# Performance work log

Hardware: AMD Instinct MI355X
Metric: run time of the kernel (lower is better)

Reference implementation:

```python
import jax, jax.numpy as jnp
import numpy as np
from jax import lax

I, H, C = 1086, 16, 15


def _lstm_layer(x, w_ih, w_hh, b):
    # x: [B, T, in], w_ih: [4H, in], w_hh: [4H, H], b: [4H]  (b = b_ih + b_hh)
    B = x.shape[0]
    Hd = w_hh.shape[1]
    # precompute the big input projection outside the scan
    pre = jnp.einsum('bti,gi->btg', x, w_ih) + b  # [B, T, 4H]

    def step(carry, pt):
        h, c = carry
        gates = pt + h @ w_hh.T  # [B, 4H]
        i, f, g, o = jnp.split(gates, 4, axis=-1)  # torch gate order i,f,g,o
        i = jax.nn.sigmoid(i)
        f = jax.nn.sigmoid(f)
        g = jnp.tanh(g)
        o = jax.nn.sigmoid(o)
        c = f * c + i * g
        h = o * jnp.tanh(c)
        return (h, c), h

    h0 = jnp.zeros((B, Hd), x.dtype)
    c0 = jnp.zeros((B, Hd), x.dtype)
    _, ys = lax.scan(step, (h0, c0), jnp.swapaxes(pre, 0, 1))
    return jnp.swapaxes(ys, 0, 1)  # [B, T, H]


def setup_inputs() -> dict:
    key = jax.random.key(0)
    ks = jax.random.split(key, 20)
    s = 1.0 / np.sqrt(H)  # torch LSTM/Linear default init scale
    x = jax.random.normal(ks[0], (256, 200, I), dtype=jnp.float32)

    def w(k, shape):
        return jax.random.uniform(k, shape, jnp.float32, -s, s)

    inp = {'x': x}
    ins = [I, H, H, H]  # lstm1 layer0/1, lstm2 layer0/1
    names = ['l0a', 'l0b', 'l1a', 'l1b']
    ki = 1
    for n, d_in in zip(names, ins):
        inp['w_ih_' + n] = w(ks[ki], (4 * H, d_in)); ki += 1
        inp['w_hh_' + n] = w(ks[ki], (4 * H, H)); ki += 1
        inp['b_' + n] = w(ks[ki], (4 * H,)); ki += 1
    inp['w_fc1'] = w(ks[ki], (H, H)); ki += 1
    inp['b_fc1'] = w(ks[ki], (H,)); ki += 1
    inp['w_fc2'] = w(ks[ki], (C, H)); ki += 1
    inp['b_fc2'] = w(ks[ki], (C,))
    return inp


def reference(x, w_ih_l0a, w_hh_l0a, b_l0a, w_ih_l0b, w_hh_l0b, b_l0b,
              w_ih_l1a, w_hh_l1a, b_l1a, w_ih_l1b, w_hh_l1b, b_l1b,
              w_fc1, b_fc1, w_fc2, b_fc2):
    # lstm1 (2 layers), dropout between layers is identity in eval mode
    out = _lstm_layer(x, w_ih_l0a, w_hh_l0a, b_l0a)
    out = _lstm_layer(out, w_ih_l0b, w_hh_l0b, b_l0b)
    # lstm2 (2 layers)
    out = _lstm_layer(out, w_ih_l1a, w_hh_l1a, b_l1a)
    out = _lstm_layer(out, w_ih_l1b, w_hh_l1b, b_l1b)
    h_last = out[:, -1, :]  # [B, H]
    h = jax.nn.relu(h_last @ w_fc1.T + b_fc1)
    logits = h @ w_fc2.T + b_fc2  # [B, C]
    return jax.nn.softmax(logits, axis=1)
```

## Files before the change

### kernel.cpp

```cpp
#include <hip/hip_runtime.h>

#define T_STEPS 200
#define IN_DIM 1086
#define KTILES 34
#define M_TOTAL 51200

using f32x4v  = __attribute__((ext_vector_type(4))) float;
using bf16x8  = __attribute__((ext_vector_type(8))) short;
using u32x4   = __attribute__((ext_vector_type(4))) unsigned int;
typedef unsigned uv2 __attribute__((ext_vector_type(2)));

#if __has_builtin(__builtin_amdgcn_permlane16_swap) && __has_builtin(__builtin_amdgcn_permlane32_swap)
#define HAVE_PERMLANE_SWAP 1
#else
#define HAVE_PERMLANE_SWAP 0
#endif

#if __has_builtin(__builtin_amdgcn_exp2f)
#define EXP2F(x) __builtin_amdgcn_exp2f(x)
#else
#define EXP2F(x) exp2f(x)
#endif

#define GLDS(gp, lp, sz) __builtin_amdgcn_global_load_lds(                         \
    (const __attribute__((address_space(1))) unsigned int*)(gp),                   \
    (__attribute__((address_space(3))) unsigned int*)(lp), sz, 0, 0)

__device__ __forceinline__ float rl_f(float v, int lane) {
    return __uint_as_float((unsigned)__builtin_amdgcn_readlane((int)__float_as_uint(v), lane));
}

__global__ __launch_bounds__(256) void prepack_w(
    const float* __restrict__ W,
    unsigned short* __restrict__ Wh, unsigned short* __restrict__ Wl)
{
    int idx = blockIdx.x * 256 + threadIdx.x;
    if (idx >= KTILES * 4 * 64 * 8) return;
    int j = idx & 7;
    int n = (idx >> 3) & 63;
    int k = (idx >> 9) * 8 + j;
    float v = (k < IN_DIM) ? W[n * IN_DIM + k] : 0.0f;
    unsigned u = __float_as_uint(v);
    unsigned hi = u & 0xffff0000u;
    float lo = v - __uint_as_float(hi);
    Wh[idx] = (unsigned short)(u >> 16);
    Wl[idx] = (unsigned short)(__float_as_uint(lo) >> 16);
}

__device__ __forceinline__ void cvt_hilo(const float (&a)[8], bf16x8& hv, bf16x8& lv) {
    union { u32x4 u; bf16x8 v; } H, L;
    #pragma unroll
    for (int p = 0; p < 4; ++p) {
        float a0 = a[2 * p], a1 = a[2 * p + 1];
        unsigned u0 = __float_as_uint(a0), u1 = __float_as_uint(a1);
        unsigned h0 = u0 & 0xffff0000u, h1 = u1 & 0xffff0000u;
        H.u[p] = (u0 >> 16) | h1;
        float l0 = a0 - __uint_as_float(h0);
        float l1 = a1 - __uint_as_float(h1);
        L.u[p] = (__float_as_uint(l0) >> 16) | (__float_as_uint(l1) & 0xffff0000u);
    }
    hv = H.v; lv = L.v;
}

__global__ __launch_bounds__(256) void pre0_gemm_v5(
    const float* __restrict__ X,
    const unsigned short* __restrict__ Wh, const unsigned short* __restrict__ Wl,
    const float* __restrict__ bias, float* __restrict__ out)
{
    __shared__ float          As[2][2048];
    __shared__ unsigned short Bs[2][2][2048];

    const int tid  = threadIdx.x;
    const int lane = tid & 63;
    const int wv   = tid >> 6;
    const int fr   = lane & 15;
    const int kg   = lane >> 4;
    const long m0  = (long)blockIdx.x * 64;

    const int rbase = wv * 16 + (lane >> 5);
    const int sidx  = (lane >> 2) & 7;
    const int dsub  = lane & 3;
    int koff[8];
    #pragma unroll
    for (int i = 0; i < 8; ++i)
        koff[i] = ((sidx ^ ((rbase + 2 * i) & 7)) * 4 + dsub) * 4;
    const char* Xrow = (const char*)X + (m0 + rbase) * 4344;

    f32x4v acc[4];
    #pragma unroll
    for (int nf = 0; nf < 4; ++nf)
        #pragma unroll
        for (int r = 0; r < 4; ++r) acc[nf][r] = 0.0f;

    {
        #pragma unroll
        for (int i = 0; i < 8; ++i) {
            int off = koff[i];
            GLDS(Xrow + (long)i * 8688 + off, &As[0][wv * 512 + i * 64], 4);
        }
        GLDS(Wh + tid * 8, (char*)Bs[0][0] + wv * 1024, 16);
        GLDS(Wl + tid * 8, (char*)Bs[0][1] + wv * 1024, 16);
    }

    for (int kt = 0; kt < KTILES; ++kt) {
        const int cur = kt & 1;
        __syncthreads();

        if (kt + 1 < KTILES) {
            const int nb = cur ^ 1, kb = (kt + 1) * 128;
            #pragma unroll
            for (int i = 0; i < 8; ++i) {
                int off = kb + koff[i];
                off = off > 4340 ? 4340 : off;
                GLDS(Xrow + (long)i * 8688 + off, &As[nb][wv * 512 + i * 64], 4);
            }
            GLDS(Wh + (size_t)(kt + 1) * 2048 + tid * 8, (char*)Bs[nb][0] + wv * 1024, 16);
            GLDS(Wl + (size_t)(kt + 1) * 2048 + tid * 8, (char*)Bs[nb][1] + wv * 1024, 16);
        }

        const int r  = wv * 16 + fr;
        const int r7 = r & 7;
        const float* pa1 = &As[cur][r * 32 + (((2 * kg) ^ r7) << 2)];
        const float* pa2 = &As[cur][r * 32 + ((((2 * kg) | 1) ^ r7) << 2)];
        float a[8];
        *(f32x4v*)&a[0] = *(const f32x4v*)pa1;
        *(f32x4v*)&a[4] = *(const f32x4v*)pa2;
        bf16x8 ah, al;
        cvt_hilo(a, ah, al);
        #pragma unroll
        for (int nf = 0; nf < 4; ++nf) {
            const int bofs = (kg * 64 + nf * 16 + fr) * 8;
            bf16x8 bh = *(const bf16x8*)&Bs[cur][0][bofs];
            bf16x8 bl = *(const bf16x8*)&Bs[cur][1][bofs];
            acc[nf] = __builtin_amdgcn_mfma_f32_16x16x32_bf16(ah, bh, acc[nf], 0, 0, 0);
            acc[nf] = __builtin_amdgcn_mfma_f32_16x16x32_bf16(al, bh, acc[nf], 0, 0, 0);
            acc[nf] = __builtin_amdgcn_mfma_f32_16x16x32_bf16(ah, bl, acc[nf], 0, 0, 0);
        }
    }

    float bvv[4];
    #pragma unroll
    for (int nf = 0; nf < 4; ++nf) bvv[nf] = bias[nf * 16 + fr];
    #pragma unroll
    for (int nf = 0; nf < 4; ++nf)
        #pragma unroll
        for (int rr = 0; rr < 4; ++rr) {
            long row = m0 + wv * 16 + kg * 4 + rr;
            out[row * 64 + nf * 16 + fr] = acc[nf][rr] + bvv[nf];
        }
}

__global__ __launch_bounds__(256) void mega_scan(
    const float* __restrict__ pre0, const float* __restrict__ whh0,
    const float* __restrict__ wih1, const float* __restrict__ whh1, const float* __restrict__ b1,
    const float* __restrict__ wih2, const float* __restrict__ whh2, const float* __restrict__ b2,
    const float* __restrict__ wih3, const float* __restrict__ whh3, const float* __restrict__ b3,
    const float* __restrict__ w_fc1, const float* __restrict__ b_fc1,
    const float* __restrict__ w_fc2, const float* __restrict__ b_fc2,
    float* __restrict__ out)
{
    __shared__ float buf[3][T_STEPS][16];

    const int b    = blockIdx.x;
    const int tid  = threadIdx.x;
    const int g    = tid & 63;
    const int wv   = tid >> 6;

    bool sel16 = false, sel32 = false;
#if HAVE_PERMLANE_SWAP
    {
        uv2 q16 = __builtin_amdgcn_permlane16_swap((unsigned)g, (unsigned)g, false, false);
        sel16 = (__builtin_amdgcn_readfirstlane((int)q16[1]) == 16);
        uv2 q32 = __builtin_amdgcn_permlane32_swap((unsigned)g, (unsigned)g, false, false);
        sel32 = (__builtin_amdgcn_readfirstlane((int)q32[1]) == 32);
    }
#endif

    const float* wih = nullptr; const float* whh; const float* bias = nullptr;
    if      (wv == 0) { whh = whh0; }
    else if (wv == 1) { wih = wih1; whh = whh1; bias = b1; }
    else if (wv == 2) { wih = wih2; whh = whh2; bias = b2; }
    else              { wih = wih3; whh = whh3; bias = b3; }

    float whh_r[16];
    #pragma unroll
    for (int q = 0; q < 4; ++q)
        *(float4*)&whh_r[q * 4] = *(const float4*)&whh[g * 16 + q * 4];
    float wih_r[16]; float bg = 0.0f;
    if (wv) {
        #pragma unroll
        for (int q = 0; q < 4; ++q)
            *(float4*)&wih_r[q * 4] = *(const float4*)&wih[g * 16 + q * 4];
        bg = bias[g];
    }

    const float* pb = pre0 + (size_t)b * T_STEPS * 64 + g;
    float pc = 0.0f, p1 = 0.0f, p2 = 0.0f;
    if (wv == 0) { pc = pb[0]; p1 = pb[64]; p2 = pb[128]; }

    float hs[16];
    #pragma unroll
    for (int k = 0; k < 16; ++k) hs[k] = 0.0f;
    float c = 0.0f;

    const int q4 = g >> 4;
    const float escale = (q4 == 2) ? -2.8853900817779268f : -1.4426950408889634f;
    const float am = (q4 == 2) ? 2.0f : 1.0f;
    const float aa = (q4 == 2) ? -1.0f : 0.0f;

    for (int tau = 0; tau < T_STEPS + 3; ++tau) {
        __syncthreads();
        const int t = tau - wv;
        if (t >= 0 && t < T_STEPS) {
            float xr[16];
            if (wv) {
                #pragma unroll
                for (int q = 0; q < 4; ++q)
                    *(float4*)&xr[q * 4] = *(const float4*)&buf[wv - 1][t][q * 4];
            }
            float r0 = fmaf(whh_r[0], hs[0], wv ? bg : pc);
            float r1 = whh_r[1] * hs[1];
            float r2 = whh_r[2] * hs[2];
            float r3 = whh_r[3] * hs[3];
            #pragma unroll
            for (int k = 4; k < 16; k += 4) {
                r0 = fmaf(whh_r[k + 0], hs[k + 0], r0);
                r1 = fmaf(whh_r[k + 1], hs[k + 1], r1);
                r2 = fmaf(whh_r[k + 2], hs[k + 2], r2);
                r3 = fmaf(whh_r[k + 3], hs[k + 3], r3);
            }
            float acc = (r0 + r1) + (r2 + r3);
            if (wv) {
                float p0 = wih_r[0] * xr[0];
                float q1 = wih_r[1] * xr[1];
                float q2 = wih_r[2] * xr[2];
                float q3 = wih_r[3] * xr[3];
                #pragma unroll
                for (int k = 4; k < 16; k += 4) {
                    p0 = fmaf(wih_r[k + 0], xr[k + 0], p0);
                    q1 = fmaf(wih_r[k + 1], xr[k + 1], q1);
                    q2 = fmaf(wih_r[k + 2], xr[k + 2], q2);
                    q3 = fmaf(wih_r[k + 3], xr[k + 3], q3);
                }
                acc += (p0 + q1) + (q2 + q3);
            }
            float e = EXP2F(escale * acc);
            float s = __builtin_amdgcn_rcpf(1.0f + e);
            float a = fmaf(am, s, aa);
#if HAVE_PERMLANE_SWAP
            unsigned au = __float_as_uint(a);
            uv2 r16 = __builtin_amdgcn_permlane16_swap(au, au, false, false);
            uv2 r32 = __builtin_amdgcn_permlane32_swap(au, au, false, false);
            unsigned fvu = sel16 ? r16[1] : r16[0];
            unsigned gvu = sel32 ? r32[1] : r32[0];
            uv2 r48 = __builtin_amdgcn_permlane16_swap(gvu, gvu, false, false);
            unsigned ovu = sel16 ? r48[1] : r48[0];
            float fv = __uint_as_float(fvu);
            float gv = __uint_as_float(gvu);
            float ov = __uint_as_float(ovu);
#else
            float fv = __shfl_xor(a, 16, 64);
            float gv = __shfl_xor(a, 32, 64);
            float ov = __shfl_xor(a, 48, 64);
#endif
            c = fmaf(fv, c, a * gv);
            float e2 = EXP2F(-2.8853900817779268f * c);
            float s2 = __builtin_amdgcn_rcpf(1.0f + e2);
            float hn = fmaf(ov + ov, s2, -ov);
            if (wv < 3 && g < 16) buf[wv][t][g] = hn;
            #pragma unroll
            for (int k = 0; k < 16; ++k) hs[k] = rl_f(hn, k);
            if (wv == 0) {
                pc = p1; p1 = p2;
                int tn = t + 3; tn = tn < T_STEPS ? tn : T_STEPS - 1;
                p2 = pb[(size_t)tn * 64];
            }
        }
    }

    if (wv == 3 && g < 16) {
        float a1 = b_fc1[g];
        #pragma unroll
        for (int k = 0; k < 16; ++k) a1 = fmaf(w_fc1[g * 16 + k], hs[k], a1);
        a1 = fmaxf(a1, 0.0f);
        float h1[16];
        #pragma unroll
        for (int k = 0; k < 16; ++k) h1[k] = rl_f(a1, k);
        float lg = -3.0e38f;
        if (g < 15) {
            lg = b_fc2[g];
            #pragma unroll
            for (int k = 0; k < 16; ++k) lg = fmaf(w_fc2[g * 16 + k], h1[k], lg);
        }
        float mx = lg;
        #pragma unroll
        for (int d = 8; d >= 1; d >>= 1) mx = fmaxf(mx, __shfl_xor(mx, d, 16));
        float ev = (g < 15) ? EXP2F(1.4426950408889634f * (lg - mx)) : 0.0f;
        float sm = ev;
        #pragma unroll
        for (int d = 8; d >= 1; d >>= 1) sm += __shfl_xor(sm, d, 16);
        if (g < 15) out[b * 15 + g] = ev * __builtin_amdgcn_rcpf(sm);
    }
}

extern "C" void kernel_launch(void* const* d_in, const int* in_sizes, int n_in,
                              void* d_out, int out_size, void* d_ws, size_t ws_size,
                              hipStream_t stream) {
    const float* x    = (const float*)d_in[0];
    const float* wih0 = (const float*)d_in[1];
    const float* whh0 = (const float*)d_in[2];
    const float* b0   = (const float*)d_in[3];
    const float* wih1 = (const float*)d_in[4];
    const float* whh1 = (const float*)d_in[5];
    const float* b1   = (const float*)d_in[6];
    const float* wih2 = (const float*)d_in[7];
    const float* whh2 = (const float*)d_in[8];
    const float* b2   = (const float*)d_in[9];
    const float* wih3 = (const float*)d_in[10];
    const float* whh3 = (const float*)d_in[11];
    const float* b3   = (const float*)d_in[12];
    const float* wfc1 = (const float*)d_in[13];
    const float* bfc1 = (const float*)d_in[14];
    const float* wfc2 = (const float*)d_in[15];
    const float* bfc2 = (const float*)d_in[16];

    float* pre0 = (float*)d_ws;
    unsigned short* Wh = (unsigned short*)((char*)d_ws + 13107200);
    unsigned short* Wl = (unsigned short*)((char*)d_ws + 13107200 + 139264);

    prepack_w<<<dim3((KTILES * 4 * 64 * 8 + 255) / 256), dim3(256), 0, stream>>>(wih0, Wh, Wl);
    pre0_gemm_v5<<<dim3(M_TOTAL / 64), dim3(256), 0, stream>>>(x, Wh, Wl, b0, pre0);
    mega_scan<<<dim3(256), dim3(256), 0, stream>>>(pre0, whh0,
        wih1, whh1, b1, wih2, whh2, b2, wih3, whh3, b3,
        wfc1, bfc1, wfc2, bfc2, (float*)d_out);
}
```

Before: 167.1 us.

## Double rows per block in input-projection GEMM with manual LDS pipeline

Each workgroup of the layer-0 input projection GEMM now handles 128 rows instead of 64, with two M fragments per wave, so every B-tile load from LDS is reused twice. The K loop is software-pipelined by hand: inline ds_read_b128, explicit vmcnt/lgkmcnt waits, raw s_barrier, and a 2x unrolled double buffer. The X-tile swizzle is redesigned and occupancy is hinted at 3 blocks per CU. The trade-off is more LDS and registers per block and half as many blocks (400) to spread across the CUs.

```diff
diff --git a/kernel.cpp b/kernel.cpp
--- a/kernel.cpp
+++ b/kernel.cpp
@@ -25,6 +25,9 @@
 #define GLDS(gp, lp, sz) __builtin_amdgcn_global_load_lds(                         \
     (const __attribute__((address_space(1))) unsigned int*)(gp),                   \
     (__attribute__((address_space(3))) unsigned int*)(lp), sz, 0, 0)
+
+#define DSR(dst, addr, off) \
+    asm volatile("ds_read_b128 %0, %1 offset:%2" : "=v"(dst) : "v"(addr), "n"(off))
 
 __device__ __forceinline__ float rl_f(float v, int lane) {
     return __uint_as_float((unsigned)__builtin_amdgcn_readlane((int)__float_as_uint(v), lane));
@@ -62,12 +65,12 @@
     hv = H.v; lv = L.v;
 }
 
-__global__ __launch_bounds__(256) void pre0_gemm_v5(
+__global__ __launch_bounds__(256, 3) void pre0_gemm_v7(
     const float* __restrict__ X,
     const unsigned short* __restrict__ Wh, const unsigned short* __restrict__ Wl,
     const float* __restrict__ bias, float* __restrict__ out)
 {
-    __shared__ float          As[2][2048];
+    __shared__ float          As[2][4096];
     __shared__ unsigned short Bs[2][2][2048];
 
     const int tid  = threadIdx.x;
@@ -75,79 +78,100 @@
     const int wv   = tid >> 6;
     const int fr   = lane & 15;
     const int kg   = lane >> 4;
-    const long m0  = (long)blockIdx.x * 64;
-
-    const int rbase = wv * 16 + (lane >> 5);
-    const int sidx  = (lane >> 2) & 7;
-    const int dsub  = lane & 3;
-    int koff[8];
-    #pragma unroll
-    for (int i = 0; i < 8; ++i)
-        koff[i] = ((sidx ^ ((rbase + 2 * i) & 7)) * 4 + dsub) * 4;
-    const char* Xrow = (const char*)X + (m0 + rbase) * 4344;
-
-    f32x4v acc[4];
-    #pragma unroll
-    for (int nf = 0; nf < 4; ++nf)
-        #pragma unroll
-        for (int r = 0; r < 4; ++r) acc[nf][r] = 0.0f;
-
-    {
-        #pragma unroll
-        for (int i = 0; i < 8; ++i) {
-            int off = koff[i];
-            GLDS(Xrow + (long)i * 8688 + off, &As[0][wv * 512 + i * 64], 4);
+    const long m0  = (long)blockIdx.x * 128;
+
+    const int d     = lane & 31;
+    const int rpar  = lane >> 5;
+    const int offE  = ((((d >> 3) ^ rpar) * 8) + (d & 7)) * 4;
+    const int offO  = ((((d >> 3) ^ (2 | rpar)) * 8) + (d & 7)) * 4;
+    const int offEc = offE > 116 ? 116 : offE;
+    const int offOc = offO > 116 ? 116 : offO;
+    const char* Px  = (const char*)X + (m0 + wv * 32 + rpar) * 4344;
+
+    const unsigned aBase = (unsigned)(unsigned long long)(void*)&As[0][0];
+    const unsigned bBase = (unsigned)(unsigned long long)(void*)&Bs[0][0][0];
+    const unsigned aAddr = aBase + (unsigned)((wv * 32 + fr) * 128 + ((kg ^ (fr & 3)) * 32));
+    const unsigned bAddr = bBase + (unsigned)((kg * 64 + fr) * 16);
+
+    f32x4v acc[2][4];
+    #pragma unroll
+    for (int mf = 0; mf < 2; ++mf)
+        #pragma unroll
+        for (int nf = 0; nf < 4; ++nf)
+            #pragma unroll
+            for (int r = 0; r < 4; ++r) acc[mf][nf][r] = 0.0f;
+
+    auto fire = [&](int kt, int nb) {
+        const int oE = (kt == 33) ? offEc : offE;
+        const int oO = (kt == 33) ? offOc : offO;
+        const char* base = Px + (long)kt * 128;
+        #pragma unroll
+        for (int i2 = 0; i2 < 16; ++i2) {
+            const char* s = base + i2 * 8688 + ((i2 & 1) ? oO : oE);
+            GLDS(s, &As[nb][(wv * 32 + 2 * i2) * 32], 4);
         }
-        GLDS(Wh + tid * 8, (char*)Bs[0][0] + wv * 1024, 16);
-        GLDS(Wl + tid * 8, (char*)Bs[0][1] + wv * 1024, 16);
-    }
-
-    for (int kt = 0; kt < KTILES; ++kt) {
-        const int cur = kt & 1;
-        __syncthreads();
-
-        if (kt + 1 < KTILES) {
-            const int nb = cur ^ 1, kb = (kt + 1) * 128;
-            #pragma unroll
-            for (int i = 0; i < 8; ++i) {
-                int off = kb + koff[i];
-                off = off > 4340 ? 4340 : off;
-                GLDS(Xrow + (long)i * 8688 + off, &As[nb][wv * 512 + i * 64], 4);
-            }
-            GLDS(Wh + (size_t)(kt + 1) * 2048 + tid * 8, (char*)Bs[nb][0] + wv * 1024, 16);
-            GLDS(Wl + (size_t)(kt + 1) * 2048 + tid * 8, (char*)Bs[nb][1] + wv * 1024, 16);
-        }
-
-        const int r  = wv * 16 + fr;
-        const int r7 = r & 7;
-        const float* pa1 = &As[cur][r * 32 + (((2 * kg) ^ r7) << 2)];
-        const float* pa2 = &As[cur][r * 32 + ((((2 * kg) | 1) ^ r7) << 2)];
-        float a[8];
-        *(f32x4v*)&a[0] = *(const f32x4v*)pa1;
-        *(f32x4v*)&a[4] = *(const f32x4v*)pa2;
-        bf16x8 ah, al;
-        cvt_hilo(a, ah, al);
-        #pragma unroll
-        for (int nf = 0; nf < 4; ++nf) {
-            const int bofs = (kg * 64 + nf * 16 + fr) * 8;
-            bf16x8 bh = *(const bf16x8*)&Bs[cur][0][bofs];
-            bf16x8 bl = *(const bf16x8*)&Bs[cur][1][bofs];
-            acc[nf] = __builtin_amdgcn_mfma_f32_16x16x32_bf16(ah, bh, acc[nf], 0, 0, 0);
-            acc[nf] = __builtin_amdgcn_mfma_f32_16x16x32_bf16(al, bh, acc[nf], 0, 0, 0);
-            acc[nf] = __builtin_amdgcn_mfma_f32_16x16x32_bf16(ah, bl, acc[nf], 0, 0, 0);
-        }
-    }
+        GLDS(Wh + (size_t)kt * 2048 + wv * 512 + lane * 8, &Bs[nb][0][wv * 512], 16);
+        GLDS(Wl + (size_t)kt * 2048 + wv * 512 + lane * 8, &Bs[nb][1][wv * 512], 16);
+    };
+
+#define GEMM_BODY(I, CUR) do {                                                     \
+    int ktn = (I) + 1; if (ktn > 33) ktn = 33;                                     \
+    fire(ktn, (CUR) ^ 1);                                                          \
+    asm volatile("s_waitcnt vmcnt(18)" ::: "memory");           \
+    __builtin_amdgcn_s_barrier();                               \
+    f32x4v a00, a01, a10, a11;                                                     \
+    bf16x8 bhv[4], blv[4];                                                         \
+    DSR(a00, aAddr, (CUR) * 16384 + 0);                                            \
+    DSR(a01, aAddr, (CUR) * 16384 + 16);                                           \
+    DSR(a10, aAddr, (CUR) * 16384 + 2048);                                         \
+    DSR(a11, aAddr, (CUR) * 16384 + 2064);                                         \
+    DSR(bhv[0], bAddr, (CUR) * 8192 + 0);                                          \
+    DSR(bhv[1], bAddr, (CUR) * 8192 + 256);                                        \
+    DSR(bhv[2], bAddr, (CUR) * 8192 + 512);                                        \
+    DSR(bhv[3], bAddr, (CUR) * 8192 + 768);                                        \
+    DSR(blv[0], bAddr, (CUR) * 8192 + 4096 + 0);                                   \
+    DSR(blv[1], bAddr, (CUR) * 8192 + 4096 + 256);                                 \
+    DSR(blv[2], bAddr, (CUR) * 8192 + 4096 + 512);                                 \
+    DSR(blv[3], bAddr, (CUR) * 8192 + 4096 + 768);                                 \
+    asm volatile("s_waitcnt lgkmcnt(0)" ::: "memory");                             \
+    __builtin_amdgcn_s_barrier();             \
+    __builtin_amdgcn_sched_barrier(0);         \
+    float a0[8] = {a00[0],a00[1],a00[2],a00[3],a01[0],a01[1],a01[2],a01[3]};       \
+    float a1[8] = {a10[0],a10[1],a10[2],a10[3],a11[0],a11[1],a11[2],a11[3]};       \
+    bf16x8 ah0, al0, ah1, al1;                                                     \
+    cvt_hilo(a0, ah0, al0);                                                        \
+    cvt_hilo(a1, ah1, al1);                                                        \
+    _Pragma("unroll")                                                              \
+    for (int nf = 0; nf < 4; ++nf) {                                               \
+        acc[0][nf] = __builtin_amdgcn_mfma_f32_16x16x32_bf16(ah0, bhv[nf], acc[0][nf], 0, 0, 0); \
+        acc[0][nf] = __builtin_amdgcn_mfma_f32_16x16x32_bf16(al0, bhv[nf], acc[0][nf], 0, 0, 0); \
+        acc[0][nf] = __builtin_amdgcn_mfma_f32_16x16x32_bf16(ah0, blv[nf], acc[0][nf], 0, 0, 0); \
+        acc[1][nf] = __builtin_amdgcn_mfma_f32_16x16x32_bf16(ah1, bhv[nf], acc[1][nf], 0, 0, 0); \
+        acc[1][nf] = __builtin_amdgcn_mfma_f32_16x16x32_bf16(al1, bhv[nf], acc[1][nf], 0, 0, 0); \
+        acc[1][nf] = __builtin_amdgcn_mfma_f32_16x16x32_bf16(ah1, blv[nf], acc[1][nf], 0, 0, 0); \
+    }                                                                              \
+} while (0)
+
+    fire(0, 0);
+    for (int i = 0; i < KTILES; i += 2) {
+        GEMM_BODY(i, 0);
+        GEMM_BODY(i + 1, 1);
+    }
+    asm volatile("s_waitcnt vmcnt(0)" ::: "memory");
+#undef GEMM_BODY
 
     float bvv[4];
     #pragma unroll
     for (int nf = 0; nf < 4; ++nf) bvv[nf] = bias[nf * 16 + fr];
     #pragma unroll
-    for (int nf = 0; nf < 4; ++nf)
-        #pragma unroll
-        for (int rr = 0; rr < 4; ++rr) {
-            long row = m0 + wv * 16 + kg * 4 + rr;
-            out[row * 64 + nf * 16 + fr] = acc[nf][rr] + bvv[nf];
-        }
+    for (int mf = 0; mf < 2; ++mf)
+        #pragma unroll
+        for (int nf = 0; nf < 4; ++nf)
+            #pragma unroll
+            for (int rr = 0; rr < 4; ++rr) {
+                long row = m0 + mf * 16 + wv * 32 + kg * 4 + rr;
+                out[row * 64 + nf * 16 + fr] = acc[mf][nf][rr] + bvv[nf];
+            }
 }
 
 __global__ __launch_bounds__(256) void mega_scan(
@@ -294,11 +318,11 @@
         }
         float mx = lg;
         #pragma unroll
-        for (int d = 8; d >= 1; d >>= 1) mx = fmaxf(mx, __shfl_xor(mx, d, 16));
+        for (int dd = 8; dd >= 1; dd >>= 1) mx = fmaxf(mx, __shfl_xor(mx, dd, 16));
         float ev = (g < 15) ? EXP2F(1.4426950408889634f * (lg - mx)) : 0.0f;
         float sm = ev;
         #pragma unroll
-        for (int d = 8; d >= 1; d >>= 1) sm += __shfl_xor(sm, d, 16);
+        for (int dd = 8; dd >= 1; dd >>= 1) sm += __shfl_xor(sm, dd, 16);
         if (g < 15) out[b * 15 + g] = ev * __builtin_amdgcn_rcpf(sm);
     }
 }
@@ -329,7 +353,7 @@
     unsigned short* Wl = (unsigned short*)((char*)d_ws + 13107200 + 139264);
 
     prepack_w<<<dim3((KTILES * 4 * 64 * 8 + 255) / 256), dim3(256), 0, stream>>>(wih0, Wh, Wl);
-    pre0_gemm_v5<<<dim3(M_TOTAL / 64), dim3(256), 0, stream>>>(x, Wh, Wl, b0, pre0);
+    pre0_gemm_v7<<<dim3(M_TOTAL / 128), dim3(256), 0, stream>>>(x, Wh, Wl, b0, pre0);
     mega_scan<<<dim3(256), dim3(256), 0, stream>>>(pre0, whh0,
         wih1, whh1, b1, wih2, whh2, b2, wih3, whh3, b3,
         wfc1, bfc1, wfc2, bfc2, (float*)d_out);
```

New measurement: 161.6 us. 3.3% less time.

## Replace LDS-staged GEMM with split-K direct global loads and LDS reduction

Applied to the files above, without the earlier changes.

The input-projection GEMM no longer stages X and the packed weights through double-buffered LDS with global_load_lds. Each block now covers 16 rows, and its four waves split the K dimension four ways, loading X and the bf16 hi/lo weights straight from global memory into registers. Partial sums are reduced through a small shared buffer at the end. This removes per-tile barriers and LDS traffic and adds blocks (with an occupancy hint), but weights are re-read per block from L2 and the X loads become narrow float2 accesses.

```diff
diff --git a/kernel.cpp b/kernel.cpp
--- a/kernel.cpp
+++ b/kernel.cpp
@@ -7,7 +7,6 @@
 
 using f32x4v  = __attribute__((ext_vector_type(4))) float;
 using bf16x8  = __attribute__((ext_vector_type(8))) short;
-using u32x4   = __attribute__((ext_vector_type(4))) unsigned int;
 typedef unsigned uv2 __attribute__((ext_vector_type(2)));
 
 #if __has_builtin(__builtin_amdgcn_permlane16_swap) && __has_builtin(__builtin_amdgcn_permlane32_swap)
@@ -21,10 +20,6 @@
 #else
 #define EXP2F(x) exp2f(x)
 #endif
-
-#define GLDS(gp, lp, sz) __builtin_amdgcn_global_load_lds(                         \
-    (const __attribute__((address_space(1))) unsigned int*)(gp),                   \
-    (__attribute__((address_space(3))) unsigned int*)(lp), sz, 0, 0)
 
 __device__ __forceinline__ float rl_f(float v, int lane) {
     return __uint_as_float((unsigned)__builtin_amdgcn_readlane((int)__float_as_uint(v), lane));
@@ -48,7 +43,7 @@
 }
 
 __device__ __forceinline__ void cvt_hilo(const float (&a)[8], bf16x8& hv, bf16x8& lv) {
-    union { u32x4 u; bf16x8 v; } H, L;
+    union { unsigned u[4]; bf16x8 v; } H, L;
     #pragma unroll
     for (int p = 0; p < 4; ++p) {
         float a0 = a[2 * p], a1 = a[2 * p + 1];
@@ -62,92 +57,78 @@
     hv = H.v; lv = L.v;
 }
 
-__global__ __launch_bounds__(256) void pre0_gemm_v5(
+__global__ __launch_bounds__(256, 8) void pre0_gemm_v10(
     const float* __restrict__ X,
     const unsigned short* __restrict__ Wh, const unsigned short* __restrict__ Wl,
     const float* __restrict__ bias, float* __restrict__ out)
 {
-    __shared__ float          As[2][2048];
-    __shared__ unsigned short Bs[2][2][2048];
+    __shared__ float red[3][64][16];
 
     const int tid  = threadIdx.x;
     const int lane = tid & 63;
-    const int wv   = tid >> 6;
+    const int wq   = tid >> 6;
     const int fr   = lane & 15;
     const int kg   = lane >> 4;
-    const long m0  = (long)blockIdx.x * 64;
-
-    const int rbase = wv * 16 + (lane >> 5);
-    const int sidx  = (lane >> 2) & 7;
-    const int dsub  = lane & 3;
-    int koff[8];
-    #pragma unroll
-    for (int i = 0; i < 8; ++i)
-        koff[i] = ((sidx ^ ((rbase + 2 * i) & 7)) * 4 + dsub) * 4;
-    const char* Xrow = (const char*)X + (m0 + rbase) * 4344;
+    const long m0  = (long)blockIdx.x * 16;
+
+    const int t0 = (wq < 2) ? wq * 9 : 18 + (wq - 2) * 8;
+    const int nt = (wq < 2) ? 9 : 8;
+
+    const float* xr = X + (m0 + fr) * (long)IN_DIM;
 
     f32x4v acc[4];
     #pragma unroll
     for (int nf = 0; nf < 4; ++nf)
         #pragma unroll
-        for (int r = 0; r < 4; ++r) acc[nf][r] = 0.0f;
-
-    {
-        #pragma unroll
-        for (int i = 0; i < 8; ++i) {
-            int off = koff[i];
-            GLDS(Xrow + (long)i * 8688 + off, &As[0][wv * 512 + i * 64], 4);
-        }
-        GLDS(Wh + tid * 8, (char*)Bs[0][0] + wv * 1024, 16);
-        GLDS(Wl + tid * 8, (char*)Bs[0][1] + wv * 1024, 16);
-    }
-
-    for (int kt = 0; kt < KTILES; ++kt) {
-        const int cur = kt & 1;
-        __syncthreads();
-
-        if (kt + 1 < KTILES) {
-            const int nb = cur ^ 1, kb = (kt + 1) * 128;
-            #pragma unroll
-            for (int i = 0; i < 8; ++i) {
-                int off = kb + koff[i];
-                off = off > 4340 ? 4340 : off;
-                GLDS(Xrow + (long)i * 8688 + off, &As[nb][wv * 512 + i * 64], 4);
-            }
-            GLDS(Wh + (size_t)(kt + 1) * 2048 + tid * 8, (char*)Bs[nb][0] + wv * 1024, 16);
-            GLDS(Wl + (size_t)(kt + 1) * 2048 + tid * 8, (char*)Bs[nb][1] + wv * 1024, 16);
-        }
-
-        const int r  = wv * 16 + fr;
-        const int r7 = r & 7;
-        const float* pa1 = &As[cur][r * 32 + (((2 * kg) ^ r7) << 2)];
-        const float* pa2 = &As[cur][r * 32 + ((((2 * kg) | 1) ^ r7) << 2)];
+        for (int q = 0; q < 4; ++q) acc[nf][q] = 0.0f;
+
+    for (int it = 0; it < nt; ++it) {
+        const int kt = t0 + it;
+        const int kb = kt * 32 + kg * 8;
         float a[8];
-        *(f32x4v*)&a[0] = *(const f32x4v*)pa1;
-        *(f32x4v*)&a[4] = *(const f32x4v*)pa2;
+        #pragma unroll
+        for (int j = 0; j < 4; ++j) {
+            const int k = kb + 2 * j;
+            float2 t;
+            if (k < IN_DIM) t = *(const float2*)(xr + k);
+            else            { t.x = 0.0f; t.y = 0.0f; }
+            a[2 * j] = t.x; a[2 * j + 1] = t.y;
+        }
         bf16x8 ah, al;
         cvt_hilo(a, ah, al);
+        const size_t bb = (size_t)(kt * 4 + kg) * 512;
         #pragma unroll
         for (int nf = 0; nf < 4; ++nf) {
-            const int bofs = (kg * 64 + nf * 16 + fr) * 8;
-            bf16x8 bh = *(const bf16x8*)&Bs[cur][0][bofs];
-            bf16x8 bl = *(const bf16x8*)&Bs[cur][1][bofs];
+            bf16x8 bh = *(const bf16x8*)(Wh + bb + (nf * 16 + fr) * 8);
+            bf16x8 bl = *(const bf16x8*)(Wl + bb + (nf * 16 + fr) * 8);
             acc[nf] = __builtin_amdgcn_mfma_f32_16x16x32_bf16(ah, bh, acc[nf], 0, 0, 0);
             acc[nf] = __builtin_amdgcn_mfma_f32_16x16x32_bf16(al, bh, acc[nf], 0, 0, 0);
             acc[nf] = __builtin_amdgcn_mfma_f32_16x16x32_bf16(ah, bl, acc[nf], 0, 0, 0);
         }
     }
 
-    float bvv[4];
-    #pragma unroll
-    for (int nf = 0; nf < 4; ++nf) bvv[nf] = bias[nf * 16 + fr];
-    #pragma unroll
-    for (int nf = 0; nf < 4; ++nf)
-        #pragma unroll
-        for (int rr = 0; rr < 4; ++rr) {
-            long row = m0 + wv * 16 + kg * 4 + rr;
-            out[row * 64 + nf * 16 + fr] = acc[nf][rr] + bvv[nf];
-        }
+    if (wq) {
+        #pragma unroll
+        for (int nf = 0; nf < 4; ++nf)
+            *(f32x4v*)&red[wq - 1][lane][nf * 4] = acc[nf];
+    }
+    __syncthreads();
+    if (wq == 0) {
+        #pragma unroll
+        for (int w = 0; w < 3; ++w)
+            #pragma unroll
+            for (int nf = 0; nf < 4; ++nf)
+                acc[nf] += *(const f32x4v*)&red[w][lane][nf * 4];
+        #pragma unroll
+        for (int nf = 0; nf < 4; ++nf) {
+            const float bv = bias[nf * 16 + fr];
+            #pragma unroll
+            for (int q = 0; q < 4; ++q) {
+                long row = m0 + kg * 4 + q;
+                out[row * 64 + nf * 16 + fr] = acc[nf][q] + bv;
+            }
+        }
+    }
 }
 
 __global__ __launch_bounds__(256) void mega_scan(
@@ -294,11 +275,11 @@
         }
         float mx = lg;
         #pragma unroll
-        for (int d = 8; d >= 1; d >>= 1) mx = fmaxf(mx, __shfl_xor(mx, d, 16));
+        for (int dd = 8; dd >= 1; dd >>= 1) mx = fmaxf(mx, __shfl_xor(mx, dd, 16));
         float ev = (g < 15) ? EXP2F(1.4426950408889634f * (lg - mx)) : 0.0f;
         float sm = ev;
         #pragma unroll
-        for (int d = 8; d >= 1; d >>= 1) sm += __shfl_xor(sm, d, 16);
+        for (int dd = 8; dd >= 1; dd >>= 1) sm += __shfl_xor(sm, dd, 16);
         if (g < 15) out[b * 15 + g] = ev * __builtin_amdgcn_rcpf(sm);
     }
 }
@@ -329,7 +310,7 @@
     unsigned short* Wl = (unsigned short*)((char*)d_ws + 13107200 + 139264);
 
     prepack_w<<<dim3((KTILES * 4 * 64 * 8 + 255) / 256), dim3(256), 0, stream>>>(wih0, Wh, Wl);
-    pre0_gemm_v5<<<dim3(M_TOTAL / 64), dim3(256), 0, stream>>>(x, Wh, Wl, b0, pre0);
+    pre0_gemm_v10<<<dim3(M_TOTAL / 16), dim3(256), 0, stream>>>(x, Wh, Wl, b0, pre0);
     mega_scan<<<dim3(256), dim3(256), 0, stream>>>(pre0, whh0,
         wih1, whh1, b1, wih2, whh2, b2, wih3, whh3, b3,
         wfc1, bfc1, wfc2, bfc2, (float*)d_out);
```

Measured after the change: 217.3 us. 30.0% more time.
